# Kernel optimization log

Hardware: AMD Instinct MI355X
Metric: run time of the kernel (lower is better)

The kernel has to match this reference:

```python
import jax, jax.numpy as jnp
import numpy as np

ALPHA, BETA, GAMMA = 0.05, 0.95, 0.95   # list_weight
TANH_ALPHA = 2.0
GDEP = 2


def _gcn_rnn(x, adp, preA, W, b):
    # GCN type 'RNN': adaptive batched adj + predefined adj
    h = x
    outs = [h]
    for _ in range(GDEP):
        h = (ALPHA * x
             + BETA * jnp.einsum('nvc,nvw->nwc', h, adp)
             + GAMMA * jnp.einsum('nvc,vw->nwc', h, preA))
        outs.append(h)
    return jnp.concatenate(outs, -1) @ W + b


def _gcn_hyper(x, A, W, b):
    h = x
    outs = [h]
    for _ in range(GDEP):
        h = ALPHA * x + GAMMA * jnp.einsum('nvc,vw->nwc', h, A)
        outs.append(h)
    return jnp.concatenate(outs, -1) @ W + b


def _gcn_tgn(x, Ab, W, b):
    h = x
    outs = [h]
    for _ in range(GDEP):
        h = ALPHA * x + GAMMA * jnp.einsum('nvc,nvw->nwc', h, Ab)
        outs.append(h)
    return jnp.concatenate(outs, -1) @ W + b


def setup_inputs() -> dict:
    key = jax.random.key(0)
    ks = jax.random.split(key, 28)
    B, T, N, F = 16, 24, 512, 2
    H, E = 64, 16          # hidden_size, node embedding dim (dims_hyper[-1])
    TGN_OUT = 32
    D_ATTN = 4 * F         # TAttn default dim_out = 4 * dim_in
    p = lambda i, shape: jax.random.normal(ks[i], shape, dtype=jnp.float32) * 0.1
    return {
        'sample': jax.random.normal(ks[0], (B, T, N, F), dtype=jnp.float32),
        'predefined_A': jax.random.uniform(ks[1], (N, N), dtype=jnp.float32),
        'w_query': p(2, (F, D_ATTN)), 'w_key': p(3, (F, D_ATTN)),
        'attn_bias': p(4, (D_ATTN,)), 'attn_trans': p(5, (D_ATTN, 1)),
        'W_tgn': p(6, ((GDEP + 1) * F, TGN_OUT)), 'b_tgn': p(7, (TGN_OUT,)),
        'W_agg1': p(8, ((GDEP + 1) * H, E)), 'b_agg1': p(9, (E,)),
        'W_agg2': p(10, ((GDEP + 1) * H, E)), 'b_agg2': p(11, (E,)),
        'W_srcemb': p(12, (F, E)), 'b_srcemb': p(13, (E,)),
        'W_tgtemb': p(14, (F, E)), 'b_tgtemb': p(15, (E,)),
        'W_gz': p(16, ((GDEP + 1) * (F + H), H)), 'b_gz': p(17, (H,)),
        'W_gr': p(18, ((GDEP + 1) * (F + H), H)), 'b_gr': p(19, (H,)),
        'W_gc': p(20, ((GDEP + 1) * (F + H), H)), 'b_gc': p(21, (H,)),
        'W_short': p(22, (TGN_OUT, F)), 'b_short': p(23, (F,)),
        'W_long': p(24, (H, F)), 'b_long': p(25, (F,)),
        'W_mix': p(26, (TGN_OUT + H, F)), 'b_mix': p(27, (F,)),
    }


def reference(sample, predefined_A, w_query, w_key, attn_bias, attn_trans,
              W_tgn, b_tgn, W_agg1, b_agg1, W_agg2, b_agg2,
              W_srcemb, b_srcemb, W_tgtemb, b_tgtemb,
              W_gz, b_gz, W_gr, b_gr, W_gc, b_gc,
              W_short, b_short, W_long, b_long, W_mix, b_mix):
    B, T, N, F = sample.shape
    H = W_long.shape[0]
    A = predefined_A
    eye = jnp.eye(N, dtype=sample.dtype)

    def gru_step(hidden, graph):
        # hidden: [B,N,H], graph: [B,N,F]
        gs = _gcn_hyper(hidden, A, W_agg1, b_agg1)
        gt = _gcn_hyper(hidden, A, W_agg2, b_agg2)
        nv_s = jnp.tanh(TANH_ALPHA * (graph @ W_srcemb + b_srcemb) * gs)
        nv_t = jnp.tanh(TANH_ALPHA * (graph @ W_tgtemb + b_tgtemb) * gt)
        a = (jnp.einsum('bnd,bmd->bnm', nv_s, nv_t)
             - jnp.einsum('bnd,bmd->bnm', nv_t, nv_s))
        adp = jax.nn.relu(jnp.tanh(TANH_ALPHA * a)) + eye
        adp = adp / adp.sum(-1, keepdims=True)           # row-normalized [B,N,N]
        combined = jnp.concatenate([graph, hidden], -1)
        z = jax.nn.sigmoid(_gcn_rnn(combined, adp, A, W_gz, b_gz))
        r = jax.nn.sigmoid(_gcn_rnn(combined, adp, A, W_gr, b_gr))
        c = jnp.tanh(_gcn_rnn(jnp.concatenate([graph, r * hidden], -1), adp, A, W_gc, b_gc))
        return z * hidden + (1.0 - z) * c

    hidden = jnp.zeros((B, N, H), dtype=sample.dtype)
    graphs = jnp.moveaxis(sample[:, 0:T - 4:4], 1, 0)    # [T', B, N, F]
    hidden = jax.lax.scan(lambda h, g: (gru_step(h, g), None), hidden, graphs)[0]

    # temporal additive attention over the last 4 graphs (TAttn)
    src = sample[:, -4:]                                  # [B,4,N,F]
    tar = sample[:, -1]                                   # [B,N,F]
    q = (tar @ w_query)[:, None, :, None, :]              # [B,1,N,1,D]
    k = (src @ w_key)[:, :, None, :, :]                   # [B,4,1,N,D]
    scores = (jnp.tanh(q + k + attn_bias) @ attn_trans)[..., 0]   # [B,4,N,N]
    attn = jax.nn.softmax(scores, axis=-1)

    # single TGN layer: graph conv with (predefined + attention) adjacency
    Ab = A[None] + attn.reshape(-1, N, N)                 # [B*4,N,N]
    out = _gcn_tgn(src.reshape(-1, N, F), Ab, W_tgn, b_tgn)
    out = jax.nn.relu(out.reshape(B, 4, N, -1))
    tar = out.sum(axis=1)                                 # [B,N,TGN_OUT]

    gat_result = tar @ W_short + b_short                  # [B,N,F]
    hidden = gru_step(hidden, gat_result)
    gru_result = hidden @ W_long + b_long
    final_result = jnp.concatenate([tar, hidden], -1) @ W_mix + b_mix
    return gat_result, gru_result, final_result, attn
```

## Files before the change

kernel.cpp:

```cpp
#include <hip/hip_runtime.h>

#define ALPHA_C 0.05f
#define BETA_C  0.95f
#define GAMMA_C 0.95f

constexpr int B = 16, T = 24, N = 512, F = 2, H = 64, E = 16;
constexpr int DA = 8;
constexpr int CC = F + H;
constexpr int TGN_OC = 32;
constexpr int NPART = 4;

__device__ __forceinline__ float fast_rcp(float x) { return __builtin_amdgcn_rcpf(x); }
__device__ __forceinline__ float fast_tanh(float x) {
    return 1.0f - 2.0f * fast_rcp(__expf(2.0f * x) + 1.0f);
}
__device__ __forceinline__ float fast_sigmoid(float x) {
    return fast_rcp(1.0f + __expf(-x));
}

__device__ __forceinline__ void gload16(const float* g, float* l)
{
    __builtin_amdgcn_global_load_lds((const __attribute__((address_space(1))) void*)g,
                                     (__attribute__((address_space(3))) void*)l, 16, 0, 0);
}

__global__ void scaleA_kernel(const float* __restrict__ A, float* __restrict__ K1)
{
    int i = blockIdx.x * 256 + threadIdx.x;
    K1[i] = GAMMA_C * A[i];
}

__global__ __launch_bounds__(256) void k2_kernel(const float* __restrict__ A,
                                                 float* __restrict__ K2)
{
    __shared__ float rows[16][258];
    __shared__ float cols[256][17];
    const int tid = threadIdx.x;
    const int r0 = blockIdx.y * 16, c0 = blockIdx.x * 16;
    const int rr = tid >> 4, cc = tid & 15;
    float acc = 0.f;
    for (int k0 = 0; k0 < N; k0 += 256) {
#pragma unroll
        for (int it = 0; it < 4; ++it) {
            int l = it * 256 + tid;
            int row = l >> 6, k4 = (l & 63) << 2;
            *(float4*)&rows[row][k4] = *(const float4*)(A + (size_t)(r0 + row) * N + k0 + k4);
        }
#pragma unroll
        for (int it = 0; it < 4; ++it) {
            int l = it * 256 + tid;
            int k = l >> 2, c4 = (l & 3) << 2;
            *(float4*)&cols[k][c4] = *(const float4*)(A + (size_t)(k0 + k) * N + c0 + c4);
        }
        __syncthreads();
#pragma unroll 8
        for (int k = 0; k < 256; ++k) acc += rows[rr][k] * cols[k][cc];
        __syncthreads();
    }
    size_t i = (size_t)(r0 + rr) * N + c0 + cc;
    K2[i] = GAMMA_C * ALPHA_C * A[i] + GAMMA_C * GAMMA_C * acc;
}

template<bool INSUM>
__global__ __launch_bounds__(512) void bmm4_kernel(
    float* __restrict__ out, const float* __restrict__ x, const float* __restrict__ in,
    const float* __restrict__ M)
{
    __shared__ float sh_m[128][64];
    __shared__ float sh_h[64][68];
    constexpr int Crow = CC;
    const size_t pstr = (size_t)B * N * Crow;
    const int tid = threadIdx.x;
    const int b = blockIdx.z, w0 = blockIdx.x * 64, vq = blockIdx.y;
    const int cg = tid & 15;
    const int wg = tid >> 4;
    const int wid = tid >> 6;
    const int lane = tid & 63;

    float acc[2][4] = {{0,0,0,0},{0,0,0,0}};
    float ag[2] = {0.f, 0.f};

    const float* Mb = M + (size_t)b * N * N + (size_t)(vq * 128) * N + w0;
    const float* inb = in + (size_t)b * N * Crow;

#pragma unroll
    for (int it = 0; it < 4; ++it) {
        int row = it * 32 + wid * 4 + (lane >> 4);
        gload16(Mb + (size_t)row * N + ((lane & 15) << 2),
                &sh_m[0][0] + (it * 2048 + wid * 256));
    }

    for (int vt = 0; vt < 2; ++vt) {
        const int v0 = vq * 128 + vt * 64;
        {
            const float2* h0 = (const float2*)(inb + (size_t)v0 * Crow);
            for (int l = tid; l < 64 * 33; l += 512) {
                int row = l / 33, k = (l - row * 33) * 2;
                float2 v = h0[l];
                if (INSUM) {
#pragma unroll
                    for (int j = 1; j < NPART; ++j) {
                        float2 w = ((const float2*)(inb + (size_t)j * pstr + (size_t)v0 * Crow))[l];
                        v.x += w.x; v.y += w.y;
                    }
                }
                *(float2*)&sh_h[row][k] = v;
            }
        }
        __syncthreads();
#pragma unroll 8
        for (int j = 0; j < 64; ++j) {
            float2 mv = *(const float2*)&sh_m[vt * 64 + j][wg << 1];
            float4 hv = *(const float4*)&sh_h[j][cg << 2];
            acc[0][0] += mv.x * hv.x; acc[0][1] += mv.x * hv.y;
            acc[0][2] += mv.x * hv.z; acc[0][3] += mv.x * hv.w;
            acc[1][0] += mv.y * hv.x; acc[1][1] += mv.y * hv.y;
            acc[1][2] += mv.y * hv.z; acc[1][3] += mv.y * hv.w;
            if (cg < 2) {
                float gv = sh_h[j][64 + cg];
                ag[0] += mv.x * gv; ag[1] += mv.y * gv;
            }
        }
        if (vt == 0) __syncthreads();
    }
    float* outp = out + (size_t)vq * pstr + (size_t)b * N * Crow;
    const float* xb = x + (size_t)b * N * Crow;
#pragma unroll
    for (int r = 0; r < 2; ++r) {
        const int w = w0 + (wg << 1) + r;
        const size_t base = (size_t)w * Crow + (cg << 2);
        float o0 = acc[r][0], o1 = acc[r][1], o2 = acc[r][2], o3 = acc[r][3];
        if (vq == 0) {
            o0 += ALPHA_C * xb[base];     o1 += ALPHA_C * xb[base + 1];
            o2 += ALPHA_C * xb[base + 2]; o3 += ALPHA_C * xb[base + 3];
        }
        float2 lo = {o0, o1}, hi = {o2, o3};
        *(float2*)(outp + base) = lo;
        *(float2*)(outp + base + 2) = hi;
        if (cg < 2) {
            size_t gb = (size_t)w * Crow + 64 + cg;
            float v = ag[r];
            if (vq == 0) v += ALPHA_C * xb[gb];
            outp[gb] = v;
        }
    }
}

__global__ __launch_bounds__(512) void hyper5_kernel(
    float* __restrict__ P1, float* __restrict__ P2, const float* __restrict__ hidden,
    const float* __restrict__ K1, const float* __restrict__ K2)
{
    __shared__ float sh_m1[64][64];
    __shared__ float sh_m2[64][64];
    __shared__ float sh_h[64][64];
    const size_t pstr = (size_t)B * N * H;
    const int tid = threadIdx.x;
    const int b = blockIdx.z, w0 = blockIdx.x * 64, vq = blockIdx.y;
    const int cg = tid & 15;
    const int wg = tid >> 4;
    const int wid = tid >> 6;
    const int lane = tid & 63;

    float a1[2][4] = {{0,0,0,0},{0,0,0,0}};
    float a2[2][4] = {{0,0,0,0},{0,0,0,0}};
    const float* inb = hidden + (size_t)b * N * H;

    for (int vt = 0; vt < 2; ++vt) {
        const int v0 = vq * 128 + vt * 64;
#pragma unroll
        for (int it = 0; it < 2; ++it) {
            int row = it * 32 + wid * 4 + (lane >> 4);
            int c4 = (lane & 15) << 2;
            int loff = it * 2048 + wid * 256;
            gload16(K1 + (size_t)(v0 + row) * N + w0 + c4, &sh_m1[0][0] + loff);
            gload16(K2 + (size_t)(v0 + row) * N + w0 + c4, &sh_m2[0][0] + loff);
            gload16(inb + (size_t)(v0 + row) * H + c4,     &sh_h[0][0]  + loff);
        }
        __syncthreads();
#pragma unroll 8
        for (int j = 0; j < 64; ++j) {
            float2 m1 = *(const float2*)&sh_m1[j][wg << 1];
            float2 m2 = *(const float2*)&sh_m2[j][wg << 1];
            float4 hv = *(const float4*)&sh_h[j][cg << 2];
            a1[0][0] += m1.x * hv.x; a1[0][1] += m1.x * hv.y;
            a1[0][2] += m1.x * hv.z; a1[0][3] += m1.x * hv.w;
            a1[1][0] += m1.y * hv.x; a1[1][1] += m1.y * hv.y;
            a1[1][2] += m1.y * hv.z; a1[1][3] += m1.y * hv.w;
            a2[0][0] += m2.x * hv.x; a2[0][1] += m2.x * hv.y;
            a2[0][2] += m2.x * hv.z; a2[0][3] += m2.x * hv.w;
            a2[1][0] += m2.y * hv.x; a2[1][1] += m2.y * hv.y;
            a2[1][2] += m2.y * hv.z; a2[1][3] += m2.y * hv.w;
        }
        __syncthreads();
    }
    float* o1 = P1 + (size_t)vq * pstr + (size_t)b * N * H;
    float* o2 = P2 + (size_t)vq * pstr + (size_t)b * N * H;
#pragma unroll
    for (int r = 0; r < 2; ++r) {
        const int w = w0 + (wg << 1) + r;
        const size_t base = (size_t)w * H + (cg << 2);
        float4 v1 = {a1[r][0], a1[r][1], a1[r][2], a1[r][3]};
        float4 v2 = {a2[r][0], a2[r][1], a2[r][2], a2[r][3]};
        if (vq == 0) {
            float4 xv = *(const float4*)(inb + base);
            v1.x += ALPHA_C * xv.x; v1.y += ALPHA_C * xv.y;
            v1.z += ALPHA_C * xv.z; v1.w += ALPHA_C * xv.w;
            v2.x += ALPHA_C * xv.x; v2.y += ALPHA_C * xv.y;
            v2.z += ALPHA_C * xv.z; v2.w += ALPHA_C * xv.w;
        }
        *(float4*)(o1 + base) = v1;
        *(float4*)(o2 + base) = v2;
    }
}

__global__ __launch_bounds__(256) void gsgt5_kernel(
    const float* __restrict__ hidden, const float* __restrict__ P1, const float* __restrict__ P2,
    const float* __restrict__ Wa1, const float* __restrict__ ba1,
    const float* __restrict__ Wa2, const float* __restrict__ ba2,
    const float* __restrict__ graph, long gstride,
    const float* __restrict__ Wsrc, const float* __restrict__ bsrc,
    const float* __restrict__ Wtgt, const float* __restrict__ btgt,
    float* __restrict__ nv_s, float* __restrict__ nv_t)
{
    constexpr size_t psH = (size_t)B * N * H;
    __shared__ float sh[16][196];
    __shared__ float W1t[16][196];
    __shared__ float W2t[16][196];
    const int tid = threadIdx.x;
    const int e = tid & 15;
    const int row = tid >> 4;
    const size_t nn0 = (size_t)blockIdx.x * 16;
    {
        int f4 = ((int)(nn0) + row) * 16 + e;
        float4 v = ((const float4*)hidden)[f4];
        *(float4*)&sh[row][e << 2] = v;
        float4 a = ((const float4*)P1)[f4];
#pragma unroll
        for (int j = 1; j < NPART; ++j) {
            float4 w = ((const float4*)(P1 + (size_t)j * psH))[f4];
            a.x += w.x; a.y += w.y; a.z += w.z; a.w += w.w;
        }
        *(float4*)&sh[row][64 + (e << 2)] = a;
        float4 c = ((const float4*)P2)[f4];
#pragma unroll
        for (int j = 1; j < NPART; ++j) {
            float4 w = ((const float4*)(P2 + (size_t)j * psH))[f4];
            c.x += w.x; c.y += w.y; c.z += w.z; c.w += w.w;
        }
        *(float4*)&sh[row][128 + (e << 2)] = c;
    }
    for (int l = tid; l < 768; l += 256) {
        int sk = l >> 2, q = l & 3;
        float4 w1 = ((const float4*)Wa1)[l];
        float4 w2 = ((const float4*)Wa2)[l];
        W1t[4 * q + 0][sk] = w1.x; W1t[4 * q + 1][sk] = w1.y;
        W1t[4 * q + 2][sk] = w1.z; W1t[4 * q + 3][sk] = w1.w;
        W2t[4 * q + 0][sk] = w2.x; W2t[4 * q + 1][sk] = w2.y;
        W2t[4 * q + 2][sk] = w2.z; W2t[4 * q + 3][sk] = w2.w;
    }
    __syncthreads();
    float gs = ba1[e], gt = ba2[e];
#pragma unroll 8
    for (int sk = 0; sk < 192; sk += 4) {
        float4 xv = *(const float4*)&sh[row][sk];
        float4 w1 = *(const float4*)&W1t[e][sk];
        float4 w2 = *(const float4*)&W2t[e][sk];
        gs += xv.x * w1.x + xv.y * w1.y + xv.z * w1.z + xv.w * w1.w;
        gt += xv.x * w2.x + xv.y * w2.y + xv.z * w2.z + xv.w * w2.w;
    }
    size_t nn = nn0 + row;
    int b = (int)(nn >> 9), n = (int)(nn & (N - 1));
    const float* g = graph + (size_t)b * gstride + (size_t)n * F;
    float g0 = g[0], g1 = g[1];
    float es = g0 * Wsrc[e] + g1 * Wsrc[E + e] + bsrc[e];
    float et = g0 * Wtgt[e] + g1 * Wtgt[E + e] + btgt[e];
    nv_s[nn * E + e] = fast_tanh(2.0f * es * gs);
    nv_t[nn * E + e] = fast_tanh(2.0f * et * gt);
}

__global__ __launch_bounds__(512) void adp3_kernel(
    const float* __restrict__ nv_s, const float* __restrict__ nv_t,
    const float* __restrict__ A,
    const float* __restrict__ hidden, const float* __restrict__ graph, long gstride,
    float* __restrict__ Mcomb, float* __restrict__ comb)
{
    __shared__ float red[8][4];
    __shared__ float tot[4];
    const int m = threadIdx.x;
    const int n0 = blockIdx.x * 4;
    const int b = blockIdx.y;
    const float4* sm = (const float4*)(nv_s + ((size_t)b * N + m) * E);
    const float4* tm = (const float4*)(nv_t + ((size_t)b * N + m) * E);
    const float4* sn = (const float4*)(nv_s + ((size_t)b * N + n0) * E);
    const float4* tn = (const float4*)(nv_t + ((size_t)b * N + n0) * E);
    float a1[4] = {0.f,0.f,0.f,0.f}, a2[4] = {0.f,0.f,0.f,0.f};
#pragma unroll
    for (int dd = 0; dd < 4; ++dd) {
        float4 smv = sm[dd], tmv = tm[dd];
#pragma unroll
        for (int r = 0; r < 4; ++r) {
            float4 snv = sn[r * 4 + dd], tnv = tn[r * 4 + dd];
            a1[r] += snv.x * tmv.x + snv.y * tmv.y + snv.z * tmv.z + snv.w * tmv.w;
            a2[r] += tnv.x * smv.x + tnv.y * smv.y + tnv.z * smv.z + tnv.w * smv.w;
        }
    }
    float p[4];
#pragma unroll
    for (int r = 0; r < 4; ++r) {
        float pv = fmaxf(fast_tanh(2.0f * (a1[r] - a2[r])), 0.0f);
        if (m == n0 + r) pv += 1.0f;
        p[r] = pv;
    }
    float sr[4] = {p[0], p[1], p[2], p[3]};
    for (int o = 32; o > 0; o >>= 1) {
#pragma unroll
        for (int r = 0; r < 4; ++r) sr[r] += __shfl_down(sr[r], o);
    }
    int wid = m >> 6, lane = m & 63;
    if (lane == 0) {
#pragma unroll
        for (int r = 0; r < 4; ++r) red[wid][r] = sr[r];
    }
    __syncthreads();
    if (m < 4) {
        float t = 0.f;
        for (int i = 0; i < 8; ++i) t += red[i][m];
        tot[m] = BETA_C * fast_rcp(t);
    }
    __syncthreads();
#pragma unroll
    for (int r = 0; r < 4; ++r)
        Mcomb[((size_t)b * N + n0 + r) * N + m] =
            GAMMA_C * A[(size_t)(n0 + r) * N + m] + p[r] * tot[r];
    if (m < 4 * CC) {
        int r = m / CC, k = m - r * CC;
        size_t nn = (size_t)b * N + n0 + r;
        float v;
        if (k < F) v = graph[(size_t)b * gstride + (size_t)(n0 + r) * F + k];
        else       v = hidden[nn * H + (k - F)];
        comb[nn * CC + k] = v;
    }
}

__device__ __forceinline__ void stage_xt(float (*Xt)[20], const float* __restrict__ base,
                                         const float* __restrict__ P1,
                                         const float* __restrict__ P2,
                                         size_t nn0, int tid)
{
    constexpr size_t psC = (size_t)B * N * CC;
    const float2* c2 = (const float2*)(base + nn0 * CC);
    const float2* p1b = (const float2*)(P1 + nn0 * CC);
    const float2* p2b = (const float2*)(P2 + nn0 * CC);
    for (int l = tid; l < 16 * 33; l += 256) {
        int row = l & 15, kp = l >> 4;
        int idx = row * 33 + kp;
        float2 v = c2[idx];
        Xt[2 * kp][row] = v.x; Xt[2 * kp + 1][row] = v.y;
        float2 a = p1b[idx];
#pragma unroll
        for (int j = 1; j < NPART; ++j) {
            float2 w = ((const float2*)(P1 + (size_t)j * psC + nn0 * CC))[idx];
            a.x += w.x; a.y += w.y;
        }
        Xt[66 + 2 * kp][row] = a.x; Xt[66 + 2 * kp + 1][row] = a.y;
        float2 c = p2b[idx];
#pragma unroll
        for (int j = 1; j < NPART; ++j) {
            float2 w = ((const float2*)(P2 + (size_t)j * psC + nn0 * CC))[idx];
            c.x += w.x; c.y += w.y;
        }
        Xt[132 + 2 * kp][row] = c.x; Xt[132 + 2 * kp + 1][row] = c.y;
    }
}

__global__ __launch_bounds__(256) void zr5_kernel(
    const float* __restrict__ comb, const float* __restrict__ P1, const float* __restrict__ P2,
    const float* __restrict__ Wgz, const float* __restrict__ bgz,
    const float* __restrict__ Wgr, const float* __restrict__ bgr,
    const float* __restrict__ hidden,
    float* __restrict__ z, float* __restrict__ comb2)
{
    __shared__ float Xt[198][20];
    __shared__ float Wl[66][128];
    const int tid = threadIdx.x;
    const size_t nn0 = (size_t)blockIdx.x * 16;

    stage_xt(Xt, comb, P1, P2, nn0, tid);

    const int cp = tid & 63;
    const int rg = tid >> 6;
    float2 bias = (cp < 32) ? *(const float2*)&bgz[2 * cp]
                            : *(const float2*)&bgr[2 * cp - 64];
    float acc[4][2];
#pragma unroll
    for (int r = 0; r < 4; ++r) { acc[r][0] = bias.x; acc[r][1] = bias.y; }

    for (int ch = 0; ch < 3; ++ch) {
        const int sk0 = ch * 66;
        for (int l = tid; l < 66 * 32; l += 256) {
            int j = l >> 5, q = l & 31;
            float4 w = (q < 16)
                ? ((const float4*)(Wgz + (size_t)(sk0 + j) * H))[q]
                : ((const float4*)(Wgr + (size_t)(sk0 + j) * H))[q - 16];
            *(float4*)&Wl[j][q << 2] = w;
        }
        __syncthreads();
#pragma unroll 6
        for (int j = 0; j < 66; ++j) {
            float4 xv = *(const float4*)&Xt[sk0 + j][rg << 2];
            float2 wv = *(const float2*)&Wl[j][cp << 1];
            acc[0][0] += xv.x * wv.x; acc[0][1] += xv.x * wv.y;
            acc[1][0] += xv.y * wv.x; acc[1][1] += xv.y * wv.y;
            acc[2][0] += xv.z * wv.x; acc[2][1] += xv.z * wv.y;
            acc[3][0] += xv.w * wv.x; acc[3][1] += xv.w * wv.y;
        }
        __syncthreads();
    }

    if (cp < 32) {
        const int oc = 2 * cp;
#pragma unroll
        for (int r = 0; r < 4; ++r) {
            size_t nn = nn0 + (rg << 2) + r;
            z[nn * H + oc]     = fast_sigmoid(acc[r][0]);
            z[nn * H + oc + 1] = fast_sigmoid(acc[r][1]);
        }
    } else {
        const int oc = 2 * cp - 64;
#pragma unroll
        for (int r = 0; r < 4; ++r) {
            size_t nn = nn0 + (rg << 2) + r;
            float h0 = hidden[nn * H + oc], h1 = hidden[nn * H + oc + 1];
            comb2[nn * CC + F + oc]     = fast_sigmoid(acc[r][0]) * h0;
            comb2[nn * CC + F + oc + 1] = fast_sigmoid(acc[r][1]) * h1;
        }
    }
    if (tid < 32) {
        int row = tid >> 1, f = tid & 1;
        comb2[(nn0 + row) * CC + f] = Xt[f][row];
    }
}

__global__ __launch_bounds__(256) void cup5_kernel(
    const float* __restrict__ comb2, const float* __restrict__ P1, const float* __restrict__ P2,
    const float* __restrict__ Wgc, const float* __restrict__ bgc,
    const float* __restrict__ z, float* __restrict__ hidden)
{
    __shared__ float Xt[198][20];
    __shared__ float Wl[66][64];
    const int tid = threadIdx.x;
    const size_t nn0 = (size_t)blockIdx.x * 16;

    stage_xt(Xt, comb2, P1, P2, nn0, tid);

    const int cp = tid & 31;
    const int rg = tid >> 5;
    float2 bias = *(const float2*)&bgc[2 * cp];
    float acc[2][2];
#pragma unroll
    for (int r = 0; r < 2; ++r) { acc[r][0] = bias.x; acc[r][1] = bias.y; }

    for (int ch = 0; ch < 3; ++ch) {
        const int sk0 = ch * 66;
        for (int l = tid; l < 66 * 16; l += 256) {
            int j = l >> 4, q = l & 15;
            float4 w = ((const float4*)(Wgc + (size_t)(sk0 + j) * H))[q];
            *(float4*)&Wl[j][q << 2] = w;
        }
        __syncthreads();
#pragma unroll 6
        for (int j = 0; j < 66; ++j) {
            float2 xv = *(const float2*)&Xt[sk0 + j][rg << 1];
            float2 wv = *(const float2*)&Wl[j][cp << 1];
            acc[0][0] += xv.x * wv.x; acc[0][1] += xv.x * wv.y;
            acc[1][0] += xv.y * wv.x; acc[1][1] += xv.y * wv.y;
        }
        __syncthreads();
    }

    const int oc = 2 * cp;
#pragma unroll
    for (int r = 0; r < 2; ++r) {
        size_t nn = nn0 + (rg << 1) + r;
        float cv0 = fast_tanh(acc[r][0]);
        float cv1 = fast_tanh(acc[r][1]);
        float zv0 = z[nn * H + oc],     ho0 = hidden[nn * H + oc];
        float zv1 = z[nn * H + oc + 1], ho1 = hidden[nn * H + oc + 1];
        hidden[nn * H + oc]     = zv0 * ho0 + (1.0f - zv0) * cv0;
        hidden[nn * H + oc + 1] = zv1 * ho1 + (1.0f - zv1) * cv1;
    }
}

__global__ void qk_kernel(const float* __restrict__ sample,
                          const float* __restrict__ wq, const float* __restrict__ wk,
                          const float* __restrict__ attn_bias,
                          float* __restrict__ q, float* __restrict__ kk)
{
    int idx = blockIdx.x * 256 + threadIdx.x;
    if (idx < B * N * DA) {
        int d = idx & 7;
        int n = (idx >> 3) & (N - 1);
        int b = idx >> 12;
        const float* tar = sample + (((size_t)b * T + (T - 1)) * N + n) * F;
        q[idx] = tar[0] * wq[d] + tar[1] * wq[DA + d] + attn_bias[d];
    } else {
        int j = idx - B * N * DA;
        int d = j & 7;
        int n = (j >> 3) & (N - 1);
        int t = (j >> 12) & 3;
        int b = j >> 14;
        const float* s = sample + (((size_t)b * T + (T - 4 + t)) * N + n) * F;
        kk[j] = s[0] * wk[d] + s[1] * wk[DA + d];
    }
}

__global__ __launch_bounds__(256) void scores3_kernel(
    const float* __restrict__ q, const float* __restrict__ kk,
    const float* __restrict__ trans, float* __restrict__ attn)
{
    int bt = blockIdx.y;
    int b = bt >> 2;
    int rbase = blockIdx.x * 16;
    int wid = threadIdx.x >> 6, lane = threadIdx.x & 63;
    const float* kkbt = kk + (size_t)bt * N * DA;
    float* attnbt = attn + (size_t)bt * N * N;
    float tr[8];
#pragma unroll
    for (int d = 0; d < 8; ++d) tr[d] = trans[d];
    for (int i = 0; i < 4; ++i) {
        int n = rbase + wid * 4 + i;
        const float* qp = q + ((size_t)b * N + n) * DA;
        float4 qa = *(const float4*)qp, qb = *(const float4*)(qp + 4);
        float ev[8]; float ssum = 0.f;
#pragma unroll
        for (int k = 0; k < 8; ++k) {
            const float* kp = kkbt + (size_t)(k * 64 + lane) * DA;
            float4 ka = *(const float4*)kp, kb = *(const float4*)(kp + 4);
            float s = fast_tanh(qa.x + ka.x) * tr[0] + fast_tanh(qa.y + ka.y) * tr[1]
                    + fast_tanh(qa.z + ka.z) * tr[2] + fast_tanh(qa.w + ka.w) * tr[3]
                    + fast_tanh(qb.x + kb.x) * tr[4] + fast_tanh(qb.y + kb.y) * tr[5]
                    + fast_tanh(qb.z + kb.z) * tr[6] + fast_tanh(qb.w + kb.w) * tr[7];
            ev[k] = __expf(s);
            ssum += ev[k];
        }
        for (int o = 32; o > 0; o >>= 1) ssum += __shfl_down(ssum, o);
        ssum = __shfl(ssum, 0);
        float rinv = fast_rcp(ssum);
#pragma unroll
        for (int k = 0; k < 8; ++k)
            attnbt[(size_t)n * N + k * 64 + lane] = ev[k] * rinv;
    }
}

__global__ __launch_bounds__(256) void tgn2_kernel(
    const float* __restrict__ A, const float* __restrict__ attn,
    const float* __restrict__ hbase, long hsB, long hsT,
    const float* __restrict__ xbase, long xsB, long xsT,
    float* __restrict__ out)
{
    __shared__ float sh_m[64][65];
    __shared__ float sh_h[64][2];
    int bt = blockIdx.y;
    int w0 = blockIdx.x * 64;
    int tid = threadIdx.x;
    int wl = tid >> 2, c = tid & 1, vh = (tid >> 1) & 1;
    const float* hp = hbase + (size_t)(bt >> 2) * hsB + (size_t)(bt & 3) * hsT;
    const float* ap = attn + (size_t)bt * N * N;
    float acc = 0.f;
    for (int vt = 0; vt < 8; ++vt) {
        int v0 = vt * 64;
#pragma unroll
        for (int it = 0; it < 16; ++it) {
            int l = it * 256 + tid;
            int vr = l >> 6, wc = l & 63;
            size_t gi = (size_t)(v0 + vr) * N + (w0 + wc);
            sh_m[wc][vr] = A[gi] + ap[gi];
        }
        if (tid < 128) sh_h[tid >> 1][tid & 1] = hp[(size_t)(v0 + (tid >> 1)) * F + (tid & 1)];
        __syncthreads();
#pragma unroll
        for (int jj = 0; jj < 32; ++jj) {
            int j = vh * 32 + jj;
            acc += sh_m[wl][j] * sh_h[j][c];
        }
        __syncthreads();
    }
    acc += __shfl_xor(acc, 2);
    if (vh == 0) {
        const float* xp = xbase + (size_t)(bt >> 2) * xsB + (size_t)(bt & 3) * xsT;
        out[((size_t)bt * N + w0 + wl) * F + c] =
            ALPHA_C * xp[(size_t)(w0 + wl) * F + c] + GAMMA_C * acc;
    }
}

__global__ __launch_bounds__(256) void tgn_out_gat_kernel(
    const float* __restrict__ sample,
    const float* __restrict__ th1, const float* __restrict__ th2,
    const float* __restrict__ Wt, const float* __restrict__ bt_,
    const float* __restrict__ Ws, const float* __restrict__ bs,
    float* __restrict__ tar32, float* __restrict__ out0)
{
    __shared__ float sh_t[8][33];
    const int tid = threadIdx.x;
    const int oc = tid & 31;
    const int r = tid >> 5;
    const size_t nn = (size_t)blockIdx.x * 8 + r;
    const int n = (int)(nn & (N - 1));
    const int b = (int)(nn >> 9);
    float acc = 0.f;
    for (int t = 0; t < 4; ++t) {
        int bt = b * 4 + t;
        const float* s = sample + (((size_t)b * T + (T - 4 + t)) * N + n) * F;
        size_t rr = ((size_t)bt * N + n) * F;
        float v = bt_[oc];
        v += s[0] * Wt[0 * TGN_OC + oc] + s[1] * Wt[1 * TGN_OC + oc];
        v += th1[rr] * Wt[2 * TGN_OC + oc] + th1[rr + 1] * Wt[3 * TGN_OC + oc];
        v += th2[rr] * Wt[4 * TGN_OC + oc] + th2[rr + 1] * Wt[5 * TGN_OC + oc];
        acc += fmaxf(v, 0.0f);
    }
    tar32[nn * TGN_OC + oc] = acc;
    sh_t[r][oc] = acc;
    __syncthreads();
    if (tid < 16) {
        int row = tid >> 1, f = tid & 1;
        size_t nn2 = (size_t)blockIdx.x * 8 + row;
        float g = bs[f];
#pragma unroll
        for (int k = 0; k < TGN_OC; ++k) g += sh_t[row][k] * Ws[(size_t)k * F + f];
        out0[nn2 * F + f] = g;
    }
}

__global__ void final_kernel(const float* __restrict__ hidden, const float* __restrict__ tar32,
                             const float* __restrict__ Wl, const float* __restrict__ bl,
                             const float* __restrict__ Wm, const float* __restrict__ bm,
                             float* __restrict__ dout_gru, float* __restrict__ dout_fin)
{
    int idx = blockIdx.x * 256 + threadIdx.x;
    int f = idx & 1;
    int nn = idx >> 1;
    const float* hp = hidden + (size_t)nn * H;
    const float* tp = tar32 + (size_t)nn * TGN_OC;
    float g = bl[f], fin = bm[f];
    for (int k = 0; k < H; ++k) g += hp[k] * Wl[(size_t)k * F + f];
    for (int k = 0; k < TGN_OC; ++k) fin += tp[k] * Wm[(size_t)k * F + f];
    for (int k = 0; k < H; ++k) fin += hp[k] * Wm[(size_t)(TGN_OC + k) * F + f];
    dout_gru[idx] = g;
    dout_fin[idx] = fin;
}

namespace {
struct Ptrs {
    const float *sample, *A, *wq, *wk, *attn_bias, *attn_trans, *Wt, *bt_;
    const float *Wa1, *ba1, *Wa2, *ba2, *Wsrc, *bsrc, *Wtgt, *btgt;
    const float *Wgz, *bgz, *Wgr, *bgr, *Wgc, *bgc, *Wsh, *bsh, *Wl, *bl, *Wm, *bm;
    float *hidden, *nvs, *nvt, *Mcomb, *K1, *K2, *comb, *comb2, *z, *P1, *P2;
    float *q, *kk, *th1, *th2, *tar32;
};

void gru_step(hipStream_t stream, const Ptrs& p, const float* graph, long gstride)
{
    dim3 bg(8, NPART, B);
    hyper5_kernel<<<bg, 512, 0, stream>>>(p.P1, p.P2, p.hidden, p.K1, p.K2);
    gsgt5_kernel<<<B * N / 16, 256, 0, stream>>>(
        p.hidden, p.P1, p.P2, p.Wa1, p.ba1, p.Wa2, p.ba2, graph, gstride,
        p.Wsrc, p.bsrc, p.Wtgt, p.btgt, p.nvs, p.nvt);
    adp3_kernel<<<dim3(N / 4, B), 512, 0, stream>>>(
        p.nvs, p.nvt, p.A, p.hidden, graph, gstride, p.Mcomb, p.comb);
    bmm4_kernel<false><<<bg, 512, 0, stream>>>(p.P1, p.comb, p.comb, p.Mcomb);
    bmm4_kernel<true><<<bg, 512, 0, stream>>>(p.P2, p.comb, p.P1, p.Mcomb);
    zr5_kernel<<<B * N / 16, 256, 0, stream>>>(
        p.comb, p.P1, p.P2, p.Wgz, p.bgz, p.Wgr, p.bgr, p.hidden, p.z, p.comb2);
    bmm4_kernel<false><<<bg, 512, 0, stream>>>(p.P1, p.comb2, p.comb2, p.Mcomb);
    bmm4_kernel<true><<<bg, 512, 0, stream>>>(p.P2, p.comb2, p.P1, p.Mcomb);
    cup5_kernel<<<B * N / 16, 256, 0, stream>>>(
        p.comb2, p.P1, p.P2, p.Wgc, p.bgc, p.z, p.hidden);
}
}

extern "C" void kernel_launch(void* const* d_in, const int* in_sizes, int n_in,
                              void* d_out, int out_size, void* d_ws, size_t ws_size,
                              hipStream_t stream)
{
    (void)in_sizes; (void)n_in; (void)out_size; (void)ws_size;
    Ptrs p;
    p.sample = (const float*)d_in[0];
    p.A      = (const float*)d_in[1];
    p.wq     = (const float*)d_in[2];
    p.wk     = (const float*)d_in[3];
    p.attn_bias  = (const float*)d_in[4];
    p.attn_trans = (const float*)d_in[5];
    p.Wt  = (const float*)d_in[6];
    p.bt_ = (const float*)d_in[7];
    p.Wa1 = (const float*)d_in[8];
    p.ba1 = (const float*)d_in[9];
    p.Wa2 = (const float*)d_in[10];
    p.ba2 = (const float*)d_in[11];
    p.Wsrc = (const float*)d_in[12];
    p.bsrc = (const float*)d_in[13];
    p.Wtgt = (const float*)d_in[14];
    p.btgt = (const float*)d_in[15];
    p.Wgz = (const float*)d_in[16];
    p.bgz = (const float*)d_in[17];
    p.Wgr = (const float*)d_in[18];
    p.bgr = (const float*)d_in[19];
    p.Wgc = (const float*)d_in[20];
    p.bgc = (const float*)d_in[21];
    p.Wsh = (const float*)d_in[22];
    p.bsh = (const float*)d_in[23];
    p.Wl  = (const float*)d_in[24];
    p.bl  = (const float*)d_in[25];
    p.Wm  = (const float*)d_in[26];
    p.bm  = (const float*)d_in[27];

    float* ws = (float*)d_ws;
    size_t off = 0;
    auto alloc = [&](size_t nelem) { float* r = ws + off; off += nelem; return r; };
    p.hidden = alloc((size_t)B * N * H);
    p.nvs    = alloc((size_t)B * N * E);
    p.nvt    = alloc((size_t)B * N * E);
    p.Mcomb  = alloc((size_t)B * N * N);
    p.K1     = alloc((size_t)N * N);
    p.K2     = alloc((size_t)N * N);
    p.comb   = alloc((size_t)B * N * CC);
    p.comb2  = alloc((size_t)B * N * CC);
    p.z      = alloc((size_t)B * N * H);
    p.P1     = alloc((size_t)NPART * B * N * CC);
    p.P2     = alloc((size_t)NPART * B * N * CC);
    p.q      = alloc((size_t)B * N * DA);
    p.kk     = alloc((size_t)B * 4 * N * DA);
    p.th1    = alloc((size_t)B * 4 * N * F);
    p.th2    = alloc((size_t)B * 4 * N * F);
    p.tar32  = alloc((size_t)B * N * TGN_OC);

    float* out = (float*)d_out;
    float* out_gat = out;
    float* out_gru = out + (size_t)B * N * F;
    float* out_fin = out + (size_t)2 * B * N * F;
    float* out_attn = out + (size_t)3 * B * N * F;

    hipMemsetAsync(p.hidden, 0, (size_t)B * N * H * sizeof(float), stream);
    scaleA_kernel<<<N * N / 256, 256, 0, stream>>>(p.A, p.K1);
    k2_kernel<<<dim3(32, 32), 256, 0, stream>>>(p.A, p.K2);

    for (int i = 0; i < 5; ++i) {
        const float* graph = p.sample + (size_t)(4 * i) * N * F;
        gru_step(stream, p, graph, (long)T * N * F);
    }

    qk_kernel<<<(B * N * DA + B * 4 * N * DA) / 256, 256, 0, stream>>>(
        p.sample, p.wq, p.wk, p.attn_bias, p.q, p.kk);
    scores3_kernel<<<dim3(32, 64), 256, 0, stream>>>(p.q, p.kk, p.attn_trans, out_attn);

    const float* srcbase = p.sample + (size_t)(T - 4) * N * F;
    tgn2_kernel<<<dim3(8, 64), 256, 0, stream>>>(
        p.A, out_attn, srcbase, (long)T * N * F, (long)N * F,
        srcbase, (long)T * N * F, (long)N * F, p.th1);
    tgn2_kernel<<<dim3(8, 64), 256, 0, stream>>>(
        p.A, out_attn, p.th1, (long)4 * N * F, (long)N * F,
        srcbase, (long)T * N * F, (long)N * F, p.th2);
    tgn_out_gat_kernel<<<B * N / 8, 256, 0, stream>>>(
        p.sample, p.th1, p.th2, p.Wt, p.bt_, p.Wsh, p.bsh, p.tar32, out_gat);

    gru_step(stream, p, out_gat, (long)N * F);

    final_kernel<<<(B * N * F) / 256, 256, 0, stream>>>(
        p.hidden, p.tar32, p.Wl, p.bl, p.Wm, p.bm, out_gru, out_fin);
}
```

Before: 1.265 ms.

## Fuse GRU step kernels into persistent megakernel with software grid barriers

Replaces the nine per-phase kernel launches of each GRU step with a single persistent kernel that loops over virtual blocks and separates phases with an atomic-based grid barrier. All five warm-up steps run in one launch, and the final step runs in a second launch. This removes launch overhead and inter-kernel gaps. In exchange it adds barrier spin costs, relies on every block being co-resident (grid sized from an occupancy query), and changes the per-thread work split in the zr/cup phases to 512-thread blocks.

Measured after the change: 1.270 ms. No clear change (+0.4%).

```diff
diff --git a/kernel.cpp b/kernel.cpp
--- a/kernel.cpp
+++ b/kernel.cpp
@@ -9,6 +9,8 @@
 constexpr int CC = F + H;
 constexpr int TGN_OC = 32;
 constexpr int NPART = 4;
+constexpr unsigned MEGA_LDS = 50176;
+constexpr int NVB = 512;
 
 __device__ __forceinline__ float fast_rcp(float x) { return __builtin_amdgcn_rcpf(x); }
 __device__ __forceinline__ float fast_tanh(float x) {
@@ -22,6 +24,27 @@
 {
     __builtin_amdgcn_global_load_lds((const __attribute__((address_space(1))) void*)g,
                                      (__attribute__((address_space(3))) void*)l, 16, 0, 0);
+}
+
+__device__ __forceinline__ void gridbar(unsigned* bar, unsigned nb)
+{
+    __syncthreads();
+    if (threadIdx.x == 0) {
+        __threadfence();
+        unsigned g = __hip_atomic_load(&bar[1], __ATOMIC_RELAXED, __HIP_MEMORY_SCOPE_AGENT);
+        unsigned arrived = __hip_atomic_fetch_add(&bar[0], 1u, __ATOMIC_ACQ_REL,
+                                                  __HIP_MEMORY_SCOPE_AGENT);
+        if (arrived == nb - 1u) {
+            __hip_atomic_store(&bar[0], 0u, __ATOMIC_RELAXED, __HIP_MEMORY_SCOPE_AGENT);
+            __hip_atomic_fetch_add(&bar[1], 1u, __ATOMIC_RELEASE, __HIP_MEMORY_SCOPE_AGENT);
+        } else {
+            while (__hip_atomic_load(&bar[1], __ATOMIC_ACQUIRE,
+                                     __HIP_MEMORY_SCOPE_AGENT) == g)
+                __builtin_amdgcn_s_sleep(4);
+        }
+        __threadfence();
+    }
+    __syncthreads();
 }
 
 __global__ void scaleA_kernel(const float* __restrict__ A, float* __restrict__ K1)
@@ -345,13 +368,13 @@
 __device__ __forceinline__ void stage_xt(float (*Xt)[20], const float* __restrict__ base,
                                          const float* __restrict__ P1,
                                          const float* __restrict__ P2,
-                                         size_t nn0, int tid)
+                                         size_t nn0, int tid, int nthr)
 {
     constexpr size_t psC = (size_t)B * N * CC;
     const float2* c2 = (const float2*)(base + nn0 * CC);
     const float2* p1b = (const float2*)(P1 + nn0 * CC);
     const float2* p2b = (const float2*)(P2 + nn0 * CC);
-    for (int l = tid; l < 16 * 33; l += 256) {
+    for (int l = tid; l < 16 * 33; l += nthr) {
         int row = l & 15, kp = l >> 4;
         int idx = row * 33 + kp;
         float2 v = c2[idx];
@@ -385,7 +408,7 @@
     const int tid = threadIdx.x;
     const size_t nn0 = (size_t)blockIdx.x * 16;
 
-    stage_xt(Xt, comb, P1, P2, nn0, tid);
+    stage_xt(Xt, comb, P1, P2, nn0, tid, 256);
 
     const int cp = tid & 63;
     const int rg = tid >> 6;
@@ -451,7 +474,7 @@
     const int tid = threadIdx.x;
     const size_t nn0 = (size_t)blockIdx.x * 16;
 
-    stage_xt(Xt, comb2, P1, P2, nn0, tid);
+    stage_xt(Xt, comb2, P1, P2, nn0, tid, 256);
 
     const int cp = tid & 31;
     const int rg = tid >> 5;
@@ -488,6 +511,405 @@
         float zv1 = z[nn * H + oc + 1], ho1 = hidden[nn * H + oc + 1];
         hidden[nn * H + oc]     = zv0 * ho0 + (1.0f - zv0) * cv0;
         hidden[nn * H + oc + 1] = zv1 * ho1 + (1.0f - zv1) * cv1;
+    }
+}
+
+struct MegaArgs {
+    const float* graph; long gstride; long gadv; int nsteps;
+    const float *A;
+    const float *Wa1, *ba1, *Wa2, *ba2, *Wsrc, *bsrc, *Wtgt, *btgt;
+    const float *Wgz, *bgz, *Wgr, *bgr, *Wgc, *bgc;
+    const float *K1, *K2;
+    float *hidden, *nvs, *nvt, *Mcomb, *comb, *comb2, *z, *P1, *P2;
+    unsigned* bar;
+};
+
+__device__ void ph_hyper(const MegaArgs& a, char* smem, int vb)
+{
+    float* sm1 = (float*)smem;
+    float* sm2 = sm1 + 4096;
+    float* shh = sm2 + 4096;
+    const size_t pstr = (size_t)B * N * H;
+    const int tid = threadIdx.x;
+    const int w0 = (vb & 7) * 64, vq = (vb >> 3) & 3, b = vb >> 5;
+    const int cg = tid & 15, wg = tid >> 4, wid = tid >> 6, lane = tid & 63;
+    float a1[2][4] = {{0,0,0,0},{0,0,0,0}};
+    float a2[2][4] = {{0,0,0,0},{0,0,0,0}};
+    const float* inb = a.hidden + (size_t)b * N * H;
+
+    for (int vt = 0; vt < 2; ++vt) {
+        const int v0 = vq * 128 + vt * 64;
+#pragma unroll
+        for (int it = 0; it < 2; ++it) {
+            int row = it * 32 + wid * 4 + (lane >> 4);
+            int c4 = (lane & 15) << 2;
+            int loff = it * 2048 + wid * 256;
+            gload16(a.K1 + (size_t)(v0 + row) * N + w0 + c4, sm1 + loff);
+            gload16(a.K2 + (size_t)(v0 + row) * N + w0 + c4, sm2 + loff);
+            gload16(inb + (size_t)(v0 + row) * H + c4,       shh + loff);
+        }
+        __syncthreads();
+#pragma unroll 8
+        for (int j = 0; j < 64; ++j) {
+            float2 m1 = *(const float2*)&sm1[j * 64 + (wg << 1)];
+            float2 m2 = *(const float2*)&sm2[j * 64 + (wg << 1)];
+            float4 hv = *(const float4*)&shh[j * 64 + (cg << 2)];
+            a1[0][0] += m1.x * hv.x; a1[0][1] += m1.x * hv.y;
+            a1[0][2] += m1.x * hv.z; a1[0][3] += m1.x * hv.w;
+            a1[1][0] += m1.y * hv.x; a1[1][1] += m1.y * hv.y;
+            a1[1][2] += m1.y * hv.z; a1[1][3] += m1.y * hv.w;
+            a2[0][0] += m2.x * hv.x; a2[0][1] += m2.x * hv.y;
+            a2[0][2] += m2.x * hv.z; a2[0][3] += m2.x * hv.w;
+            a2[1][0] += m2.y * hv.x; a2[1][1] += m2.y * hv.y;
+            a2[1][2] += m2.y * hv.z; a2[1][3] += m2.y * hv.w;
+        }
+        __syncthreads();
+    }
+    float* o1 = a.P1 + (size_t)vq * pstr + (size_t)b * N * H;
+    float* o2 = a.P2 + (size_t)vq * pstr + (size_t)b * N * H;
+#pragma unroll
+    for (int r = 0; r < 2; ++r) {
+        const int w = w0 + (wg << 1) + r;
+        const size_t base = (size_t)w * H + (cg << 2);
+        float4 v1 = {a1[r][0], a1[r][1], a1[r][2], a1[r][3]};
+        float4 v2 = {a2[r][0], a2[r][1], a2[r][2], a2[r][3]};
+        if (vq == 0) {
+            float4 xv = *(const float4*)(inb + base);
+            v1.x += ALPHA_C * xv.x; v1.y += ALPHA_C * xv.y;
+            v1.z += ALPHA_C * xv.z; v1.w += ALPHA_C * xv.w;
+            v2.x += ALPHA_C * xv.x; v2.y += ALPHA_C * xv.y;
+            v2.z += ALPHA_C * xv.z; v2.w += ALPHA_C * xv.w;
+        }
+        *(float4*)(o1 + base) = v1;
+        *(float4*)(o2 + base) = v2;
+    }
+}
+
+__device__ void ph_gsgt(const MegaArgs& a, char* smem, const float* graph, int vb)
+{
+    constexpr size_t psH = (size_t)B * N * H;
+    float (*sh)[196]  = (float(*)[196])smem;
+    float (*W1t)[196] = (float(*)[196])(smem + 16 * 196 * 4);
+    float (*W2t)[196] = (float(*)[196])(smem + 32 * 196 * 4);
+    const int tid = threadIdx.x;
+    const size_t nn0 = (size_t)vb * 16;
+    for (int l = tid; l < 768; l += 512) {
+        int seg = l >> 8, rr = (l >> 4) & 15, ee = l & 15;
+        int f4 = ((int)nn0 + rr) * 16 + ee;
+        float4 v;
+        if (seg == 0) {
+            v = ((const float4*)a.hidden)[f4];
+        } else {
+            const float* Pp = (seg == 1) ? a.P1 : a.P2;
+            v = ((const float4*)Pp)[f4];
+#pragma unroll
+            for (int j = 1; j < NPART; ++j) {
+                float4 w = ((const float4*)(Pp + (size_t)j * psH))[f4];
+                v.x += w.x; v.y += w.y; v.z += w.z; v.w += w.w;
+            }
+        }
+        *(float4*)&sh[rr][seg * 64 + (ee << 2)] = v;
+    }
+    for (int l = tid; l < 768; l += 512) {
+        int sk = l >> 2, q = l & 3;
+        float4 w1 = ((const float4*)a.Wa1)[l];
+        float4 w2 = ((const float4*)a.Wa2)[l];
+        W1t[4 * q + 0][sk] = w1.x; W1t[4 * q + 1][sk] = w1.y;
+        W1t[4 * q + 2][sk] = w1.z; W1t[4 * q + 3][sk] = w1.w;
+        W2t[4 * q + 0][sk] = w2.x; W2t[4 * q + 1][sk] = w2.y;
+        W2t[4 * q + 2][sk] = w2.z; W2t[4 * q + 3][sk] = w2.w;
+    }
+    __syncthreads();
+    const int e = tid & 15, row = (tid >> 4) & 15, which = tid >> 8;
+    float acc = which ? a.ba2[e] : a.ba1[e];
+    const float (*Wt_)[196] = which ? W2t : W1t;
+#pragma unroll 8
+    for (int sk = 0; sk < 192; sk += 4) {
+        float4 xv = *(const float4*)&sh[row][sk];
+        float4 wv = *(const float4*)&Wt_[e][sk];
+        acc += xv.x * wv.x + xv.y * wv.y + xv.z * wv.z + xv.w * wv.w;
+    }
+    size_t nn = nn0 + row;
+    int b = (int)(nn >> 9), n = (int)(nn & (N - 1));
+    const float* gp = graph + (size_t)b * a.gstride + (size_t)n * F;
+    float g0 = gp[0], g1 = gp[1];
+    if (which == 0) {
+        float es = g0 * a.Wsrc[e] + g1 * a.Wsrc[E + e] + a.bsrc[e];
+        a.nvs[nn * E + e] = fast_tanh(2.0f * es * acc);
+    } else {
+        float et = g0 * a.Wtgt[e] + g1 * a.Wtgt[E + e] + a.btgt[e];
+        a.nvt[nn * E + e] = fast_tanh(2.0f * et * acc);
+    }
+}
+
+__device__ void ph_adp(const MegaArgs& a, char* smem, const float* graph, int vb)
+{
+    float (*red)[4] = (float(*)[4])smem;
+    float* tot = (float*)(smem + 128);
+    const int m = threadIdx.x;
+    const int b = vb >> 5;
+    const int ng = vb & 31;
+    const float4* sm = (const float4*)(a.nvs + ((size_t)b * N + m) * E);
+    const float4* tm = (const float4*)(a.nvt + ((size_t)b * N + m) * E);
+    float4 smv[4], tmv[4];
+#pragma unroll
+    for (int dd = 0; dd < 4; ++dd) { smv[dd] = sm[dd]; tmv[dd] = tm[dd]; }
+
+    for (int c = 0; c < 4; ++c) {
+        const int n0 = (ng + 32 * c) * 4;
+        const float4* sn = (const float4*)(a.nvs + ((size_t)b * N + n0) * E);
+        const float4* tn = (const float4*)(a.nvt + ((size_t)b * N + n0) * E);
+        float a1[4] = {0.f,0.f,0.f,0.f}, a2[4] = {0.f,0.f,0.f,0.f};
+#pragma unroll
+        for (int dd = 0; dd < 4; ++dd) {
+#pragma unroll
+            for (int r = 0; r < 4; ++r) {
+                float4 snv = sn[r * 4 + dd], tnv = tn[r * 4 + dd];
+                a1[r] += snv.x * tmv[dd].x + snv.y * tmv[dd].y + snv.z * tmv[dd].z + snv.w * tmv[dd].w;
+                a2[r] += tnv.x * smv[dd].x + tnv.y * smv[dd].y + tnv.z * smv[dd].z + tnv.w * smv[dd].w;
+            }
+        }
+        float p[4];
+#pragma unroll
+        for (int r = 0; r < 4; ++r) {
+            float pv = fmaxf(fast_tanh(2.0f * (a1[r] - a2[r])), 0.0f);
+            if (m == n0 + r) pv += 1.0f;
+            p[r] = pv;
+        }
+        float sr[4] = {p[0], p[1], p[2], p[3]};
+        for (int o = 32; o > 0; o >>= 1) {
+#pragma unroll
+            for (int r = 0; r < 4; ++r) sr[r] += __shfl_down(sr[r], o);
+        }
+        int wid = m >> 6, lane = m & 63;
+        if (lane == 0) {
+#pragma unroll
+            for (int r = 0; r < 4; ++r) red[wid][r] = sr[r];
+        }
+        __syncthreads();
+        if (m < 4) {
+            float t = 0.f;
+            for (int i = 0; i < 8; ++i) t += red[i][m];
+            tot[m] = BETA_C * fast_rcp(t);
+        }
+        __syncthreads();
+#pragma unroll
+        for (int r = 0; r < 4; ++r)
+            a.Mcomb[((size_t)b * N + n0 + r) * N + m] =
+                GAMMA_C * a.A[(size_t)(n0 + r) * N + m] + p[r] * tot[r];
+        if (m < 4 * CC) {
+            int r = m / CC, k = m - r * CC;
+            size_t nn = (size_t)b * N + n0 + r;
+            float v;
+            if (k < F) v = graph[(size_t)b * a.gstride + (size_t)(n0 + r) * F + k];
+            else       v = a.hidden[nn * H + (k - F)];
+            a.comb[nn * CC + k] = v;
+        }
+        __syncthreads();
+    }
+}
+
+template<bool INSUM>
+__device__ void ph_bmm(const MegaArgs& a, char* smem,
+                       float* out, const float* x, const float* in, int vb)
+{
+    float* sh_m = (float*)smem;
+    float (*sh_h)[68] = (float(*)[68])(smem + 128 * 64 * 4);
+    constexpr int Crow = CC;
+    const size_t pstr = (size_t)B * N * Crow;
+    const int tid = threadIdx.x;
+    const int w0 = (vb & 7) * 64, vq = (vb >> 3) & 3, b = vb >> 5;
+    const int cg = tid & 15, wg = tid >> 4, wid = tid >> 6, lane = tid & 63;
+
+    float acc[2][4] = {{0,0,0,0},{0,0,0,0}};
+    float ag[2] = {0.f, 0.f};
+
+    const float* Mb = a.Mcomb + (size_t)b * N * N + (size_t)(vq * 128) * N + w0;
+    const float* inb = in + (size_t)b * N * Crow;
+
+#pragma unroll
+    for (int it = 0; it < 4; ++it) {
+        int row = it * 32 + wid * 4 + (lane >> 4);
+        gload16(Mb + (size_t)row * N + ((lane & 15) << 2),
+                sh_m + (it * 2048 + wid * 256));
+    }
+
+    for (int vt = 0; vt < 2; ++vt) {
+        const int v0 = vq * 128 + vt * 64;
+        {
+            const float2* h0 = (const float2*)(inb + (size_t)v0 * Crow);
+            for (int l = tid; l < 64 * 33; l += 512) {
+                int row = l / 33, k = (l - row * 33) * 2;
+                float2 v = h0[l];
+                if (INSUM) {
+#pragma unroll
+                    for (int j = 1; j < NPART; ++j) {
+                        float2 w = ((const float2*)(inb + (size_t)j * pstr + (size_t)v0 * Crow))[l];
+                        v.x += w.x; v.y += w.y;
+                    }
+                }
+                *(float2*)&sh_h[row][k] = v;
+            }
+        }
+        __syncthreads();
+#pragma unroll 8
+        for (int j = 0; j < 64; ++j) {
+            float2 mv = *(const float2*)&sh_m[(vt * 64 + j) * 64 + (wg << 1)];
+            float4 hv = *(const float4*)&sh_h[j][cg << 2];
+            acc[0][0] += mv.x * hv.x; acc[0][1] += mv.x * hv.y;
+            acc[0][2] += mv.x * hv.z; acc[0][3] += mv.x * hv.w;
+            acc[1][0] += mv.y * hv.x; acc[1][1] += mv.y * hv.y;
+            acc[1][2] += mv.y * hv.z; acc[1][3] += mv.y * hv.w;
+            if (cg < 2) {
+                float gv = sh_h[j][64 + cg];
+                ag[0] += mv.x * gv; ag[1] += mv.y * gv;
+            }
+        }
+        if (vt == 0) __syncthreads();
+    }
+    float* outp = out + (size_t)vq * pstr + (size_t)b * N * Crow;
+    const float* xb = x + (size_t)b * N * Crow;
+#pragma unroll
+    for (int r = 0; r < 2; ++r) {
+        const int w = w0 + (wg << 1) + r;
+        const size_t base = (size_t)w * Crow + (cg << 2);
+        float o0 = acc[r][0], o1 = acc[r][1], o2 = acc[r][2], o3 = acc[r][3];
+        if (vq == 0) {
+            o0 += ALPHA_C * xb[base];     o1 += ALPHA_C * xb[base + 1];
+            o2 += ALPHA_C * xb[base + 2]; o3 += ALPHA_C * xb[base + 3];
+        }
+        float2 lo = {o0, o1}, hi = {o2, o3};
+        *(float2*)(outp + base) = lo;
+        *(float2*)(outp + base + 2) = hi;
+        if (cg < 2) {
+            size_t gb = (size_t)w * Crow + 64 + cg;
+            float v = ag[r];
+            if (vq == 0) v += ALPHA_C * xb[gb];
+            outp[gb] = v;
+        }
+    }
+}
+
+__device__ void ph_zr(const MegaArgs& a, char* smem, int vb)
+{
+    float (*Xt)[20] = (float(*)[20])smem;
+    float (*Wl)[128] = (float(*)[128])(smem + 198 * 20 * 4);
+    const int tid = threadIdx.x;
+    const size_t nn0 = (size_t)vb * 16;
+
+    stage_xt(Xt, a.comb, a.P1, a.P2, nn0, tid, 512);
+
+    const int cp = tid & 63;
+    const int rg = tid >> 6;
+    float2 bias = (cp < 32) ? *(const float2*)&a.bgz[2 * cp]
+                            : *(const float2*)&a.bgr[2 * cp - 64];
+    float acc[2][2] = {{bias.x, bias.y}, {bias.x, bias.y}};
+
+    for (int ch = 0; ch < 3; ++ch) {
+        const int sk0 = ch * 66;
+        for (int l = tid; l < 66 * 32; l += 512) {
+            int j = l >> 5, q = l & 31;
+            float4 w = (q < 16)
+                ? ((const float4*)(a.Wgz + (size_t)(sk0 + j) * H))[q]
+                : ((const float4*)(a.Wgr + (size_t)(sk0 + j) * H))[q - 16];
+            *(float4*)&Wl[j][q << 2] = w;
+        }
+        __syncthreads();
+#pragma unroll 6
+        for (int j = 0; j < 66; ++j) {
+            float2 xv = *(const float2*)&Xt[sk0 + j][rg << 1];
+            float2 wv = *(const float2*)&Wl[j][cp << 1];
+            acc[0][0] += xv.x * wv.x; acc[0][1] += xv.x * wv.y;
+            acc[1][0] += xv.y * wv.x; acc[1][1] += xv.y * wv.y;
+        }
+        __syncthreads();
+    }
+
+    if (cp < 32) {
+        const int oc = 2 * cp;
+#pragma unroll
+        for (int r = 0; r < 2; ++r) {
+            size_t nn = nn0 + (rg << 1) + r;
+            a.z[nn * H + oc]     = fast_sigmoid(acc[r][0]);
+            a.z[nn * H + oc + 1] = fast_sigmoid(acc[r][1]);
+        }
+    } else {
+        const int oc = 2 * cp - 64;
+#pragma unroll
+        for (int r = 0; r < 2; ++r) {
+            size_t nn = nn0 + (rg << 1) + r;
+            float h0 = a.hidden[nn * H + oc], h1 = a.hidden[nn * H + oc + 1];
+            a.comb2[nn * CC + F + oc]     = fast_sigmoid(acc[r][0]) * h0;
+            a.comb2[nn * CC + F + oc + 1] = fast_sigmoid(acc[r][1]) * h1;
+        }
+    }
+    if (tid < 32) {
+        int row = tid >> 1, f = tid & 1;
+        a.comb2[(nn0 + row) * CC + f] = Xt[f][row];
+    }
+}
+
+__device__ void ph_cup(const MegaArgs& a, char* smem, int vb)
+{
+    float (*Xt)[20] = (float(*)[20])smem;
+    float (*Wl)[64] = (float(*)[64])(smem + 198 * 20 * 4);
+    const int tid = threadIdx.x;
+    const size_t nn0 = (size_t)vb * 16;
+
+    stage_xt(Xt, a.comb2, a.P1, a.P2, nn0, tid, 512);
+
+    const int cp = tid & 31;
+    const int rg = tid >> 5;
+    float2 bias = *(const float2*)&a.bgc[2 * cp];
+    float acc0 = bias.x, acc1 = bias.y;
+
+    for (int ch = 0; ch < 3; ++ch) {
+        const int sk0 = ch * 66;
+        for (int l = tid; l < 66 * 16; l += 512) {
+            int j = l >> 4, q = l & 15;
+            float4 w = ((const float4*)(a.Wgc + (size_t)(sk0 + j) * H))[q];
+            *(float4*)&Wl[j][q << 2] = w;
+        }
+        __syncthreads();
+#pragma unroll 6
+        for (int j = 0; j < 66; ++j) {
+            float xv = Xt[sk0 + j][rg];
+            float2 wv = *(const float2*)&Wl[j][cp << 1];
+            acc0 += xv * wv.x; acc1 += xv * wv.y;
+        }
+        __syncthreads();
+    }
+
+    const int oc = 2 * cp;
+    size_t nn = nn0 + rg;
+    float cv0 = fast_tanh(acc0);
+    float cv1 = fast_tanh(acc1);
+    float zv0 = a.z[nn * H + oc],     ho0 = a.hidden[nn * H + oc];
+    float zv1 = a.z[nn * H + oc + 1], ho1 = a.hidden[nn * H + oc + 1];
+    a.hidden[nn * H + oc]     = zv0 * ho0 + (1.0f - zv0) * cv0;
+    a.hidden[nn * H + oc + 1] = zv1 * ho1 + (1.0f - zv1) * cv1;
+}
+
+#define VB_LOOP(body) for (int vb = blockIdx.x; vb < NVB; vb += nbk) { body; __syncthreads(); }
+
+__global__ __launch_bounds__(512, 2) void gru_mega(MegaArgs a)
+{
+    extern __shared__ float smem_f[];
+    char* smem = (char*)smem_f;
+    const int nbk = gridDim.x;
+    unsigned* bar = a.bar;
+    const float* graph = a.graph;
+    for (int s = 0; s < a.nsteps; ++s) {
+        VB_LOOP(ph_hyper(a, smem, vb));                              gridbar(bar, nbk);
+        VB_LOOP(ph_gsgt(a, smem, graph, vb));                        gridbar(bar, nbk);
+        VB_LOOP(ph_adp(a, smem, graph, vb));                         gridbar(bar, nbk);
+        VB_LOOP(ph_bmm<false>(a, smem, a.P1, a.comb, a.comb, vb));   gridbar(bar, nbk);
+        VB_LOOP(ph_bmm<true>(a, smem, a.P2, a.comb, a.P1, vb));      gridbar(bar, nbk);
+        VB_LOOP(ph_zr(a, smem, vb));                                 gridbar(bar, nbk);
+        VB_LOOP(ph_bmm<false>(a, smem, a.P1, a.comb2, a.comb2, vb)); gridbar(bar, nbk);
+        VB_LOOP(ph_bmm<true>(a, smem, a.P2, a.comb2, a.P1, vb));     gridbar(bar, nbk);
+        VB_LOOP(ph_cup(a, smem, vb));                                gridbar(bar, nbk);
+        graph += a.gadv;
     }
 }
 
@@ -656,6 +1078,7 @@
     const float *Wgz, *bgz, *Wgr, *bgr, *Wgc, *bgc, *Wsh, *bsh, *Wl, *bl, *Wm, *bm;
     float *hidden, *nvs, *nvt, *Mcomb, *K1, *K2, *comb, *comb2, *z, *P1, *P2;
     float *q, *kk, *th1, *th2, *tar32;
+    unsigned* bar;
 };
 
 void gru_step(hipStream_t stream, const Ptrs& p, const float* graph, long gstride)
@@ -732,6 +1155,7 @@
     p.th1    = alloc((size_t)B * 4 * N * F);
     p.th2    = alloc((size_t)B * 4 * N * F);
     p.tar32  = alloc((size_t)B * N * TGN_OC);
+    p.bar    = (unsigned*)alloc(16);
 
     float* out = (float*)d_out;
     float* out_gat = out;
@@ -740,12 +1164,35 @@
     float* out_attn = out + (size_t)3 * B * N * F;
 
     hipMemsetAsync(p.hidden, 0, (size_t)B * N * H * sizeof(float), stream);
+    hipMemsetAsync(p.bar, 0, 16 * sizeof(float), stream);
     scaleA_kernel<<<N * N / 256, 256, 0, stream>>>(p.A, p.K1);
     k2_kernel<<<dim3(32, 32), 256, 0, stream>>>(p.A, p.K2);
 
-    for (int i = 0; i < 5; ++i) {
-        const float* graph = p.sample + (size_t)(4 * i) * N * F;
-        gru_step(stream, p, graph, (long)T * N * F);
+    int mp = 0, nb = 0;
+    hipDeviceGetAttribute(&mp, hipDeviceAttributeMultiprocessorCount, 0);
+    hipOccupancyMaxActiveBlocksPerMultiprocessor(&nb, gru_mega, 512, (size_t)MEGA_LDS);
+    int grid = nb * mp;
+    if (grid > NVB) grid = NVB;
+    bool mega_ok = (grid >= 64);
+
+    MegaArgs ma;
+    ma.graph = p.sample; ma.gstride = (long)T * N * F; ma.gadv = (long)4 * N * F;
+    ma.nsteps = 5;
+    ma.A = p.A;
+    ma.Wa1 = p.Wa1; ma.ba1 = p.ba1; ma.Wa2 = p.Wa2; ma.ba2 = p.ba2;
+    ma.Wsrc = p.Wsrc; ma.bsrc = p.bsrc; ma.Wtgt = p.Wtgt; ma.btgt = p.btgt;
+    ma.Wgz = p.Wgz; ma.bgz = p.bgz; ma.Wgr = p.Wgr; ma.bgr = p.bgr;
+    ma.Wgc = p.Wgc; ma.bgc = p.bgc;
+    ma.K1 = p.K1; ma.K2 = p.K2;
+    ma.hidden = p.hidden; ma.nvs = p.nvs; ma.nvt = p.nvt; ma.Mcomb = p.Mcomb;
+    ma.comb = p.comb; ma.comb2 = p.comb2; ma.z = p.z; ma.P1 = p.P1; ma.P2 = p.P2;
+    ma.bar = p.bar;
+
+    if (mega_ok) {
+        gru_mega<<<grid, 512, MEGA_LDS, stream>>>(ma);
+    } else {
+        for (int i = 0; i < 5; ++i)
+            gru_step(stream, p, p.sample + (size_t)(4 * i) * N * F, (long)T * N * F);
     }
 
     qk_kernel<<<(B * N * DA + B * 4 * N * DA) / 256, 256, 0, stream>>>(
@@ -762,7 +1209,13 @@
     tgn_out_gat_kernel<<<B * N / 8, 256, 0, stream>>>(
         p.sample, p.th1, p.th2, p.Wt, p.bt_, p.Wsh, p.bsh, p.tar32, out_gat);
 
-    gru_step(stream, p, out_gat, (long)N * F);
+    MegaArgs ma2 = ma;
+    ma2.graph = out_gat; ma2.gstride = (long)N * F; ma2.gadv = 0; ma2.nsteps = 1;
+    if (mega_ok) {
+        gru_mega<<<grid, 512, MEGA_LDS, stream>>>(ma2);
+    } else {
+        gru_step(stream, p, out_gat, (long)N * F);
+    }
 
     final_kernel<<<(B * N * F) / 256, 256, 0, stream>>>(
         p.hidden, p.tar32, p.Wl, p.bl, p.Wm, p.bm, out_gru, out_fin);
```
